# Kernel tuning notes

Hardware: AMD Instinct MI355X
Metric: run time of the kernel (lower is better)

The kernel has to match this reference:

```python
import jax, jax.numpy as jnp
import numpy as np
from jax import lax

N_NODES = 4000
N_IN = 32
N_OUT = 32
T = 2048
CONNECTIVITY = 0.1
SPECTRAL_RADIUS = 0.9
INPUT_SCALING = 0.5
FEEDBACK_SCALING = 0.5
LEAK = 0.99  # leaking_rate[0]; leaking_rate[1] = 1 - LEAK


def setup_inputs() -> dict:
    key = jax.random.key(0)
    ks = jax.random.split(key, 8)
    # Sparse reservoir: uniform(-1,1) weights kept with prob=connectivity
    accept = jax.random.uniform(ks[0], (N_NODES, N_NODES)) < CONNECTIVITY
    W = (jax.random.uniform(ks[1], (N_NODES, N_NODES)) * 2.0 - 1.0) * accept
    # Rescale to target spectral radius via power iteration (done once, host-side)
    W_np = np.asarray(W, dtype=np.float64)
    v = np.ones(N_NODES)
    for _ in range(60):
        v = W_np @ v
        v = v / (np.linalg.norm(v) + 1e-12)
    rho = float(np.linalg.norm(W_np @ v))
    W_res = (W * (SPECTRAL_RADIUS / max(rho, 1e-6))).astype(jnp.float32)
    W_in = ((jax.random.uniform(ks[2], (N_NODES, N_IN)) * 2 - 1) * INPUT_SCALING).astype(jnp.float32)
    W_fb = ((jax.random.uniform(ks[3], (N_NODES, N_OUT)) * 2 - 1) * FEEDBACK_SCALING).astype(jnp.float32)
    b = jnp.zeros((), dtype=jnp.float32)  # bias=0 default
    W_out = (jax.random.normal(ks[4], (N_OUT, N_IN + N_NODES)) * 0.02).astype(jnp.float32)
    X = jax.random.normal(ks[5], (T, N_IN), dtype=jnp.float32)
    y = jax.random.normal(ks[6], (T, N_OUT), dtype=jnp.float32)
    return {"X": X, "y": y, "W_in": W_in, "W_res": W_res, "W_fb": W_fb, "W_out": W_out, "b": b}


def reference(X, y, W_in, W_res, W_fb, W_out, b):
    # Sequential leaky-integrator reservoir update (train_state), noise=0.
    # h_{t+1} = LEAK * tanh(W_in x_t + b + W_res h_t + W_fb y_t) + (1-LEAK) * h_t
    inp_proj = X @ W_in.T   # [T, N] precompute input drive
    fb_proj = y @ W_fb.T    # [T, N] teacher-forced feedback drive

    def step(h, drive):
        pre = drive + b + W_res @ h
        h_new = LEAK * jnp.tanh(pre) + (1.0 - LEAK) * h
        return h_new, h_new

    h0 = jnp.zeros((N_NODES,), dtype=X.dtype)
    _, states = lax.scan(step, h0, inp_proj + fb_proj)  # states: [T, N]
    # forward(): LinOut on extended states cat([X, state])
    extended = jnp.concatenate([X, states], axis=1)     # [T, N_IN + N]
    out = extended @ W_out.T                            # [T, N_OUT]
    return out
```

## Files before the change

### kernel.cpp

```cpp
#include <hip/hip_runtime.h>
#include <hip/hip_bf16.h>

#define T_STEPS 2048
#define NN 4000
#define N_IN 32
#define N_OUT 32
#define NEXT 4032
#define NWG 250
#define ROWS_PER_WG 16
#define TPB 256
#define MAX_NNZ 7680
#define LEAK 0.99f
#define TAG_STRIDE 16

__global__ void drive_kernel(const float* __restrict__ X, const float* __restrict__ y,
                             const float* __restrict__ W_in, const float* __restrict__ W_fb,
                             const float* __restrict__ b, float* __restrict__ drive) {
  __shared__ float s_x[N_IN];
  __shared__ float s_y[N_OUT];
  const int t = blockIdx.y;
  const int tid = threadIdx.x;
  if (tid < N_IN) s_x[tid] = X[t * N_IN + tid];
  else if (tid < N_IN + N_OUT) s_y[tid - N_IN] = y[t * N_OUT + (tid - N_IN)];
  __syncthreads();
  const int n = blockIdx.x * TPB + tid;
  if (n < NN) {
    float acc = b[0];
    const float* wi = W_in + (size_t)n * N_IN;
    const float* wf = W_fb + (size_t)n * N_OUT;
#pragma unroll
    for (int k = 0; k < N_IN; ++k) acc += s_x[k] * wi[k];
#pragma unroll
    for (int k = 0; k < N_OUT; ++k) acc += s_y[k] * wf[k];
    drive[(size_t)t * NN + n] = acc;
  }
}

__global__ void transpose_wout_kernel(const float* __restrict__ W_out, float* __restrict__ WoT) {
  const int idx = blockIdx.x * TPB + threadIdx.x;
  if (idx < N_OUT * NEXT) {
    const int o = idx / NEXT;
    const int k = idx % NEXT;
    WoT[k * N_OUT + o] = W_out[idx];
  }
}

__global__ __launch_bounds__(TPB, 1) void esn_scan_kernel(
    const float* __restrict__ W_res,
    const float* __restrict__ drive,
    float* __restrict__ states,
    unsigned* __restrict__ tags) {
  __shared__ float2 s_pk[MAX_NNZ];
  __shared__ __align__(16) float s_h[NN];
  __shared__ unsigned s_cnt[ROWS_PER_WG];
  __shared__ unsigned s_start[ROWS_PER_WG + 1];

  const int tid = threadIdx.x;
  const int wg = blockIdx.x;
  const int row0 = wg * ROWS_PER_WG;
  const int wave = tid >> 6;
  const int lane = tid & 63;

  for (int rl = 0; rl < 4; ++rl) {
    const int r = wave * 4 + rl;
    const float* wrow = W_res + (size_t)(row0 + r) * NN;
    unsigned cnt = 0;
    for (int c0 = 0; c0 < NN; c0 += 64) {
      const int c = c0 + lane;
      const float w = (c < NN) ? wrow[c] : 0.0f;
      cnt += (unsigned)__popcll(__ballot(w != 0.0f));
    }
    if (lane == 0) s_cnt[r] = cnt;
  }
  __syncthreads();
  if (tid == 0) {
    unsigned acc = 0;
    for (int r = 0; r < ROWS_PER_WG; ++r) { s_start[r] = acc; acc += s_cnt[r]; }
    s_start[ROWS_PER_WG] = acc;
  }
  __syncthreads();

  for (int rl = 0; rl < 4; ++rl) {
    const int r = wave * 4 + rl;
    const float* wrow = W_res + (size_t)(row0 + r) * NN;
    unsigned off = s_start[r];
    for (int c0 = 0; c0 < NN; c0 += 64) {
      const int c = c0 + lane;
      const float w = (c < NN) ? wrow[c] : 0.0f;
      const unsigned long long m = __ballot(w != 0.0f);
      if (w != 0.0f) {
        const unsigned pos = off + (unsigned)__popcll(m & ((1ULL << lane) - 1ULL));
        if (pos < MAX_NNZ) s_pk[pos] = make_float2(w, __uint_as_float((unsigned)c));
      }
      off += (unsigned)__popcll(m);
    }
  }

  for (int i = tid; i < NN; i += TPB) s_h[i] = 0.0f;
  __syncthreads();

  const int r = tid >> 4;
  const int l16 = tid & 15;
  const int myrow = row0 + r;
  const unsigned kbeg = s_start[r];
  const unsigned kend = s_start[r + 1];

  const int p = (tid < NWG) ? (tid + wg) % NWG : 0;
  const int jrot = tid & 7;

  float dv = (l16 == 0) ? drive[myrow] : 0.0f;

  for (int t = 0; t < T_STEPS; ++t) {
    float acc0 = 0.0f, acc1 = 0.0f;
    unsigned k = kbeg + (unsigned)l16;
    for (; k + 16 < kend; k += 32) {
      const float2 p0 = s_pk[k];
      const float2 p1 = s_pk[k + 16];
      acc0 += p0.x * s_h[__float_as_uint(p0.y)];
      acc1 += p1.x * s_h[__float_as_uint(p1.y)];
    }
    if (k < kend) { const float2 pk = s_pk[k]; acc0 += pk.x * s_h[__float_as_uint(pk.y)]; }
    float acc = acc0 + acc1;
    acc += __shfl_xor(acc, 1);
    acc += __shfl_xor(acc, 2);
    acc += __shfl_xor(acc, 4);
    acc += __shfl_xor(acc, 8);

    const float dv_next = (l16 == 0 && t + 1 < T_STEPS)
                              ? drive[(size_t)(t + 1) * NN + myrow] : 0.0f;

    if (l16 == 0) {
      const float hn = LEAK * tanhf(acc + dv) + (1.0f - LEAK) * s_h[myrow];
      __hip_atomic_store(&states[(size_t)t * NN + myrow], hn,
                         __ATOMIC_RELAXED, __HIP_MEMORY_SCOPE_AGENT);
    }
    dv = dv_next;
    if (t == T_STEPS - 1) break;

    const unsigned tgt = (unsigned)(t + 1);

    asm volatile("s_waitcnt vmcnt(0)" ::: "memory");
    __syncthreads();
    if (tid == 0) {
      __hip_atomic_store(&tags[wg * TAG_STRIDE], tgt, __ATOMIC_RELAXED,
                         __HIP_MEMORY_SCOPE_AGENT);
    }

    if (tid < NWG) {
      while (__hip_atomic_load(&tags[p * TAG_STRIDE], __ATOMIC_RELAXED,
                               __HIP_MEMORY_SCOPE_AGENT) < tgt)
        __builtin_amdgcn_s_sleep(1);
      const unsigned long long* src =
          (const unsigned long long*)(states + (size_t)t * NN + p * 16);
      unsigned long long* dst = (unsigned long long*)&s_h[p * 16];
#pragma unroll
      for (int jj = 0; jj < 8; ++jj) {
        const int j = (jrot + jj) & 7;
        dst[j] = __hip_atomic_load(&src[j], __ATOMIC_RELAXED,
                                   __HIP_MEMORY_SCOPE_AGENT);
      }
    }
    __syncthreads();
  }
}

__global__ void out_kernel(const float* __restrict__ X, const float* __restrict__ states,
                           const float* __restrict__ WoT, float* __restrict__ out) {
  const int o = threadIdx.x & 31;
  const int tl = threadIdx.x >> 5;
  const int t = blockIdx.x * 8 + tl;
  float acc = 0.0f;
  const float* xrow = X + (size_t)t * N_IN;
#pragma unroll
  for (int k = 0; k < N_IN; ++k) acc += xrow[k] * WoT[k * N_OUT + o];
  const float* srow = states + (size_t)t * NN;
  for (int j = 0; j < NN; ++j) acc += srow[j] * WoT[(N_IN + j) * N_OUT + o];
  out[(size_t)t * N_OUT + o] = acc;
}

extern "C" void kernel_launch(void* const* d_in, const int* in_sizes, int n_in,
                              void* d_out, int out_size, void* d_ws, size_t ws_size,
                              hipStream_t stream) {
  const float* X     = (const float*)d_in[0];
  const float* y     = (const float*)d_in[1];
  const float* W_in  = (const float*)d_in[2];
  const float* W_res = (const float*)d_in[3];
  const float* W_fb  = (const float*)d_in[4];
  const float* W_out = (const float*)d_in[5];
  const float* b     = (const float*)d_in[6];
  float* out = (float*)d_out;

  float* ws = (float*)d_ws;
  float* drive    = ws;
  float* states   = ws + 8192000;
  float* WoT      = ws + 16384000;
  unsigned* tags  = (unsigned*)(ws + 16513024);

  hipMemsetAsync(tags, 0, 4096 * sizeof(unsigned), stream);
  drive_kernel<<<dim3(16, T_STEPS), TPB, 0, stream>>>(X, y, W_in, W_fb, b, drive);
  transpose_wout_kernel<<<(N_OUT * NEXT + TPB - 1) / TPB, TPB, 0, stream>>>(W_out, WoT);
  esn_scan_kernel<<<NWG, TPB, 0, stream>>>(W_res, drive, states, tags);
  out_kernel<<<T_STEPS / 8, TPB, 0, stream>>>(X, states, WoT, out);
}
```

Before: 9.996 ms.

## Replace per-workgroup tag flags with tagged value-plus-step words for inter-WG exchange

```diff
diff --git a/kernel.cpp b/kernel.cpp
--- a/kernel.cpp
+++ b/kernel.cpp
@@ -11,7 +11,6 @@
 #define TPB 256
 #define MAX_NNZ 7680
 #define LEAK 0.99f
-#define TAG_STRIDE 16
 
 __global__ void drive_kernel(const float* __restrict__ X, const float* __restrict__ y,
                              const float* __restrict__ W_in, const float* __restrict__ W_fb,
@@ -49,7 +48,7 @@
     const float* __restrict__ W_res,
     const float* __restrict__ drive,
     float* __restrict__ states,
-    unsigned* __restrict__ tags) {
+    unsigned long long* __restrict__ pdata) {
   __shared__ float2 s_pk[MAX_NNZ];
   __shared__ __align__(16) float s_h[NN];
   __shared__ unsigned s_cnt[ROWS_PER_WG];
@@ -106,7 +105,7 @@
   const unsigned kend = s_start[r + 1];
 
   const int p = (tid < NWG) ? (tid + wg) % NWG : 0;
-  const int jrot = tid & 7;
+  const int jrot = tid & 15;
 
   float dv = (l16 == 0) ? drive[myrow] : 0.0f;
 
@@ -129,35 +128,42 @@
     const float dv_next = (l16 == 0 && t + 1 < T_STEPS)
                               ? drive[(size_t)(t + 1) * NN + myrow] : 0.0f;
 
+    const unsigned tgt = (unsigned)(t + 1);
+    float hn = 0.0f;
     if (l16 == 0) {
-      const float hn = LEAK * tanhf(acc + dv) + (1.0f - LEAK) * s_h[myrow];
+      hn = LEAK * tanhf(acc + dv) + (1.0f - LEAK) * s_h[myrow];
+      const unsigned long long pk =
+          ((unsigned long long)tgt << 32) | (unsigned long long)__float_as_uint(hn);
+      __hip_atomic_store(&pdata[(size_t)(t & 1) * NN + myrow], pk,
+                         __ATOMIC_RELAXED, __HIP_MEMORY_SCOPE_AGENT);
       __hip_atomic_store(&states[(size_t)t * NN + myrow], hn,
                          __ATOMIC_RELAXED, __HIP_MEMORY_SCOPE_AGENT);
     }
     dv = dv_next;
     if (t == T_STEPS - 1) break;
 
-    const unsigned tgt = (unsigned)(t + 1);
-
-    asm volatile("s_waitcnt vmcnt(0)" ::: "memory");
     __syncthreads();
-    if (tid == 0) {
-      __hip_atomic_store(&tags[wg * TAG_STRIDE], tgt, __ATOMIC_RELAXED,
-                         __HIP_MEMORY_SCOPE_AGENT);
-    }
-
-    if (tid < NWG) {
-      while (__hip_atomic_load(&tags[p * TAG_STRIDE], __ATOMIC_RELAXED,
-                               __HIP_MEMORY_SCOPE_AGENT) < tgt)
+
+    if (l16 == 0) s_h[myrow] = hn;
+
+    if (tid < NWG && p != wg) {
+      const unsigned long long* src = pdata + (size_t)(t & 1) * NN + (size_t)p * 16;
+      unsigned long long v[16];
+      for (;;) {
+        bool ok = true;
+#pragma unroll
+        for (int j = 0; j < 16; ++j) {
+          v[j] = __hip_atomic_load(&src[j], __ATOMIC_RELAXED,
+                                   __HIP_MEMORY_SCOPE_AGENT);
+          ok &= ((unsigned)(v[j] >> 32) >= tgt);
+        }
+        if (ok) break;
         __builtin_amdgcn_s_sleep(1);
-      const unsigned long long* src =
-          (const unsigned long long*)(states + (size_t)t * NN + p * 16);
-      unsigned long long* dst = (unsigned long long*)&s_h[p * 16];
-#pragma unroll
-      for (int jj = 0; jj < 8; ++jj) {
-        const int j = (jrot + jj) & 7;
-        dst[j] = __hip_atomic_load(&src[j], __ATOMIC_RELAXED,
-                                   __HIP_MEMORY_SCOPE_AGENT);
+      }
+#pragma unroll
+      for (int jj = 0; jj < 16; ++jj) {
+        const int j = (jj + jrot) & 15;
+        s_h[p * 16 + j] = __uint_as_float((unsigned)v[j]);
       }
     }
     __syncthreads();
@@ -194,11 +200,11 @@
   float* drive    = ws;
   float* states   = ws + 8192000;
   float* WoT      = ws + 16384000;
-  unsigned* tags  = (unsigned*)(ws + 16513024);
-
-  hipMemsetAsync(tags, 0, 4096 * sizeof(unsigned), stream);
+  unsigned long long* pdata = (unsigned long long*)(ws + 16513024);
+
+  hipMemsetAsync(pdata, 0, 2 * NN * sizeof(unsigned long long), stream);
   drive_kernel<<<dim3(16, T_STEPS), TPB, 0, stream>>>(X, y, W_in, W_fb, b, drive);
   transpose_wout_kernel<<<(N_OUT * NEXT + TPB - 1) / TPB, TPB, 0, stream>>>(W_out, WoT);
-  esn_scan_kernel<<<NWG, TPB, 0, stream>>>(W_res, drive, states, tags);
+  esn_scan_kernel<<<NWG, TPB, 0, stream>>>(W_res, drive, states, pdata);
   out_kernel<<<T_STEPS / 8, TPB, 0, stream>>>(X, states, WoT, out);
 }
```

After: 20.07 ms. +100.8%, slower.
